# Kernel tuning notes

Hardware: AMD Instinct MI355X
Metric: run time of the kernel (lower is better)

The kernel has to match this reference:

```python
import jax, jax.numpy as jnp
import numpy as np
import math

# Model config (matches init_kwargs)
V, D, H, L, DFF, S_MAX = 32000, 512, 8, 6, 2048, 1024
DK = D // H


def _layernorm(x, g, b, eps=1e-5):
    m = jnp.mean(x, axis=-1, keepdims=True)
    v = jnp.mean(jnp.square(x - m), axis=-1, keepdims=True)
    return (x - m) / jnp.sqrt(v + eps) * g + b


def _pos_encoding(seq_len, d_model):
    # sin on even dims, cos on odd dims
    pos = jnp.arange(seq_len, dtype=jnp.float32)[:, None]          # [S,1]
    div = jnp.exp(jnp.arange(0, d_model, 2, dtype=jnp.float32) *
                  (-math.log(10000.0) / d_model))                   # [D/2]
    ang = pos * div                                                 # [S,D/2]
    pe = jnp.stack([jnp.sin(ang), jnp.cos(ang)], axis=-1)           # [S,D/2,2]
    return pe.reshape(seq_len, d_model)                             # [S,D]


def setup_inputs() -> dict:
    key = jax.random.key(0)
    ks = jax.random.split(key, 24)
    sd = 0.02

    def n(k, shape):
        return jax.random.normal(k, shape, jnp.float32) * sd

    B, S = 2, 1024
    return {
        "tokens": jax.random.randint(ks[0], (B, S), 0, V, dtype=jnp.int32),
        "tok_emb": n(ks[1], (V, D)),
        # attention projections, [L, D, D] stored as (in, out)
        "Wq": n(ks[2], (L, D, D)), "bq": jnp.zeros((L, D)),
        "Wk": n(ks[3], (L, D, D)), "bk": jnp.zeros((L, D)),
        "Wv": n(ks[4], (L, D, D)), "bv": jnp.zeros((L, D)),
        "Wo": n(ks[5], (L, D, D)), "bo": jnp.zeros((L, D)),
        "ln1_g": jnp.ones((L, D)), "ln1_b": jnp.zeros((L, D)),
        "W1": n(ks[6], (L, D, DFF)), "b1": jnp.zeros((L, DFF)),
        "W2": n(ks[7], (L, DFF, D)), "b2": jnp.zeros((L, D)),
        "ln2_g": jnp.ones((L, D)), "ln2_b": jnp.zeros((L, D)),
        "lnf_g": jnp.ones((D,)), "lnf_b": jnp.zeros((D,)),
        "Wout": n(ks[8], (D, V)), "bout": jnp.zeros((V,)),
    }


def reference(tokens, tok_emb, Wq, bq, Wk, bk, Wv, bv, Wo, bo,
              ln1_g, ln1_b, W1, b1, W2, b2, ln2_g, ln2_b,
              lnf_g, lnf_b, Wout, bout):
    B, S = tokens.shape
    x = tok_emb[tokens] * math.sqrt(D) + _pos_encoding(S, D)[None]   # [B,S,D]
    causal = jnp.tril(jnp.ones((S, S), dtype=bool))[None, None]       # [1,1,S,S]
    scale = math.sqrt(DK)

    attns = []
    for l in range(L):
        q = (x @ Wq[l] + bq[l]).reshape(B, S, H, DK).transpose(0, 2, 1, 3)
        k = (x @ Wk[l] + bk[l]).reshape(B, S, H, DK).transpose(0, 2, 1, 3)
        v = (x @ Wv[l] + bv[l]).reshape(B, S, H, DK).transpose(0, 2, 1, 3)
        scores = jnp.einsum('bhsk,bhtk->bhst', q, k) / scale           # [B,H,S,S]
        scores = jnp.where(causal, scores, -1e9)
        a = jax.nn.softmax(scores, axis=-1)
        ctx = jnp.einsum('bhst,bhtk->bhsk', a, v)                      # [B,H,S,DK]
        ctx = ctx.transpose(0, 2, 1, 3).reshape(B, S, D)
        attn_out = ctx @ Wo[l] + bo[l]
        x = _layernorm(x + attn_out, ln1_g[l], ln1_b[l])
        h = jax.nn.gelu(x @ W1[l] + b1[l], approximate=False)          # torch GELU (exact)
        ff = h @ W2[l] + b2[l]
        x = _layernorm(x + ff, ln2_g[l], ln2_b[l])
        attns.append(a)

    x = _layernorm(x, lnf_g, lnf_b)
    logits = x @ Wout + bout                                           # [B,S,V]
    return logits, jnp.stack(attns)                                    # attn: [L,B,H,S,S]
```

## Files before the change

### kernel.cpp

```cpp
#include <hip/hip_runtime.h>
#include <math.h>

#define NB 2
#define NS 1024
#define NH 8
#define NDK 64
#define ND 512
#define NDFF 2048
#define NV 32000
#define NL 6
#define MROWS (NB * NS)
#define QKVLD (3 * ND)

using bf16_t = __bf16;
using bf16x4 = __attribute__((ext_vector_type(4))) __bf16;
using bf16x8 = __attribute__((ext_vector_type(8))) __bf16;
using f32x4  = __attribute__((ext_vector_type(4))) float;

__device__ __forceinline__ void gload_lds16(const bf16_t* g, bf16_t* l) {
  __builtin_amdgcn_global_load_lds(
      (const __attribute__((address_space(1))) void*)g,
      (__attribute__((address_space(3))) void*)l, 16, 0, 0);
}

__device__ __forceinline__ float gelu_exact(float v) {
  return 0.5f * v * (1.0f + erff(v * 0.7071067811865476f));
}

__global__ __launch_bounds__(256)
void prep_kernel(const int* __restrict__ tokens, const float* __restrict__ emb,
                 const float* __restrict__ Wq, const float* __restrict__ Wk,
                 const float* __restrict__ Wv, const float* __restrict__ Wo,
                 const float* __restrict__ W1, const float* __restrict__ W2,
                 const float* __restrict__ Wout,
                 bf16_t* __restrict__ WqkvT, bf16_t* __restrict__ WoT,
                 bf16_t* __restrict__ W1T, bf16_t* __restrict__ W2T,
                 bf16_t* __restrict__ WoutT,
                 float* __restrict__ x, bf16_t* __restrict__ xb) {
  __shared__ bf16_t T[64][72];
  const int id = blockIdx.x;
  const int tid = threadIdx.x;

  if (id >= 8608) {
    const int row = id - 8608;
    const int s = row & (NS - 1);
    const int tok = tokens[row];
    const float SQRTD = 22.627416997969522f;
    const float C = -9.210340371976184f / (float)ND;
#pragma unroll
    for (int i = 0; i < 2; ++i) {
      const int d = tid + i * 256;
      const int pair = d >> 1;
      const float div = expf((float)(2 * pair) * C);
      const float ang = (float)s * div;
      const float pe = (d & 1) ? cosf(ang) : sinf(ang);
      const float v = emb[(size_t)tok * ND + d] * SQRTD + pe;
      x[(size_t)row * ND + d] = v;
      xb[(size_t)row * ND + d] = (bf16_t)v;
    }
    return;
  }

  const float* src; bf16_t* dst; int K, N, n0, k0;
  if (id < 1536) {
    const int z = id >> 6, t = id & 63;
    const int mat = z / 6, layer = z % 6;
    src = ((mat == 0) ? Wq : (mat == 1) ? Wk : (mat == 2) ? Wv : Wo) + (size_t)layer * ND * ND;
    dst = (mat < 3) ? (WqkvT + (size_t)layer * QKVLD * ND + (size_t)mat * ND * ND)
                    : (WoT + (size_t)layer * ND * ND);
    K = ND; N = ND; n0 = (t & 7) * 64; k0 = (t >> 3) * 64;
  } else if (id < 3072) {
    const int idx = id - 1536, layer = idx >> 8, t = idx & 255;
    src = W1 + (size_t)layer * ND * NDFF; dst = W1T + (size_t)layer * NDFF * ND;
    K = ND; N = NDFF; n0 = (t & 31) * 64; k0 = (t >> 5) * 64;
  } else if (id < 4608) {
    const int idx = id - 3072, layer = idx >> 8, t = idx & 255;
    src = W2 + (size_t)layer * NDFF * ND; dst = W2T + (size_t)layer * ND * NDFF;
    K = NDFF; N = ND; n0 = (t & 7) * 64; k0 = (t >> 3) * 64;
  } else {
    const int t = id - 4608;
    src = Wout; dst = WoutT;
    K = ND; N = NV; n0 = (t % 500) * 64; k0 = (t / 500) * 64;
  }

#pragma unroll
  for (int it = 0; it < 4; ++it) {
    const int k = (tid >> 4) + it * 16;
    const int c = (tid & 15) * 4;
    const float4 v = *(const float4*)&src[(size_t)(k0 + k) * N + n0 + c];
    T[c + 0][k] = (bf16_t)v.x;
    T[c + 1][k] = (bf16_t)v.y;
    T[c + 2][k] = (bf16_t)v.z;
    T[c + 3][k] = (bf16_t)v.w;
  }
  __syncthreads();
  const int n = tid >> 2, kk = (tid & 3) * 16;
  bf16x8 a = *(const bf16x8*)&T[n][kk];
  bf16x8 b2v = *(const bf16x8*)&T[n][kk + 8];
  *(bf16x8*)&dst[(size_t)(n0 + n) * K + k0 + kk] = a;
  *(bf16x8*)&dst[(size_t)(n0 + n) * K + k0 + kk + 8] = b2v;
}

__global__ __launch_bounds__(256)
void add_ln_kernel(float* __restrict__ x, const float* __restrict__ y0,
                   const float* __restrict__ y1,
                   const float* __restrict__ g, const float* __restrict__ bb,
                   const float* __restrict__ g2, const float* __restrict__ bb2,
                   bf16_t* __restrict__ xb) {
  const int row = blockIdx.x, tid = threadIdx.x;
  const size_t base = (size_t)row * ND;
  float v0 = x[base + tid], v1 = x[base + tid + 256];
  if (y0) { v0 += y0[base + tid]; v1 += y0[base + tid + 256]; }
  if (y1) { v0 += y1[base + tid]; v1 += y1[base + tid + 256]; }
  __shared__ float red[256];
  red[tid] = v0 + v1; __syncthreads();
  for (int o = 128; o > 0; o >>= 1) {
    if (tid < o) red[tid] += red[tid + o];
    __syncthreads();
  }
  const float mean = red[0] * (1.f / (float)ND);
  __syncthreads();
  const float d0 = v0 - mean, d1 = v1 - mean;
  red[tid] = d0 * d0 + d1 * d1; __syncthreads();
  for (int o = 128; o > 0; o >>= 1) {
    if (tid < o) red[tid] += red[tid + o];
    __syncthreads();
  }
  const float inv = 1.f / sqrtf(red[0] * (1.f / (float)ND) + 1e-5f);
  float o0 = d0 * inv * g[tid]       + bb[tid];
  float o1 = d1 * inv * g[tid + 256] + bb[tid + 256];

  if (g2) {
    __syncthreads();
    red[tid] = o0 + o1; __syncthreads();
    for (int o = 128; o > 0; o >>= 1) {
      if (tid < o) red[tid] += red[tid + o];
      __syncthreads();
    }
    const float mean2 = red[0] * (1.f / (float)ND);
    __syncthreads();
    const float e0 = o0 - mean2, e1 = o1 - mean2;
    red[tid] = e0 * e0 + e1 * e1; __syncthreads();
    for (int o = 128; o > 0; o >>= 1) {
      if (tid < o) red[tid] += red[tid + o];
      __syncthreads();
    }
    const float inv2 = 1.f / sqrtf(red[0] * (1.f / (float)ND) + 1e-5f);
    o0 = e0 * inv2 * g2[tid]       + bb2[tid];
    o1 = e1 * inv2 * g2[tid + 256] + bb2[tid + 256];
  } else {
    x[base + tid] = o0;
    x[base + tid + 256] = o1;
  }
  xb[base + tid] = (bf16_t)o0; xb[base + tid + 256] = (bf16_t)o1;
}

template <int ACT, int OUTBF>
__global__ __launch_bounds__(256)
void gemm_bt(const bf16_t* __restrict__ A, const bf16_t* __restrict__ Wt,
             const float* __restrict__ B0,
             void* __restrict__ Cout, int N, int K, int lda, int ldc) {
  __shared__ bf16_t As[128 * 64];
  __shared__ bf16_t Bs[128 * 64];
  const int tid = threadIdx.x, lane = tid & 63, w = tid >> 6;
  const int wm = w >> 1, wn = w & 1;
  const int lcol = lane & 15, hi = lane >> 4;

  const int nwg = gridDim.x * gridDim.y;
  const int flat = blockIdx.y * gridDim.x + blockIdx.x;
  const int q = nwg >> 3, r = nwg & 7;
  const int xcd = flat & 7, idx = flat >> 3;
  const int nf = (xcd < r ? xcd * (q + 1) : r * (q + 1) + (xcd - r) * q) + idx;
  const int m0 = (nf % gridDim.x) * 128, n0 = (nf / gridDim.x) * 128;

  const int sr8 = lane >> 3;
  const int sslot = lane & 7;

  f32x4 acc[4][4] = {};

  for (int k0 = 0; k0 < K; k0 += 64) {
#pragma unroll
    for (int t = 0; t < 2; ++t) {
#pragma unroll
      for (int c = 0; c < 2; ++c) {
        const int rbase = t * 64 + w * 16 + c * 8;
        const int row = rbase + sr8;
        const int ks = sslot ^ (row & 7);
        gload_lds16(&A[(size_t)(m0 + row) * lda + k0 + ks * 8], &As[rbase * 64]);
        gload_lds16(&Wt[(size_t)(n0 + row) * K + k0 + ks * 8], &Bs[rbase * 64]);
      }
    }
    __syncthreads();

#pragma unroll
    for (int kk = 0; kk < 2; ++kk) {
      bf16x8 af[4], bf[4];
#pragma unroll
      for (int m = 0; m < 4; ++m) {
        const int rr = wm * 64 + m * 16 + lcol;
        af[m] = *(const bf16x8*)&As[rr * 64 + (((kk * 4 + hi) ^ (rr & 7)) * 8)];
      }
#pragma unroll
      for (int n = 0; n < 4; ++n) {
        const int rr = wn * 64 + n * 16 + lcol;
        bf[n] = *(const bf16x8*)&Bs[rr * 64 + (((kk * 4 + hi) ^ (rr & 7)) * 8)];
      }
#pragma unroll
      for (int m = 0; m < 4; ++m)
#pragma unroll
        for (int n = 0; n < 4; ++n)
          acc[m][n] = __builtin_amdgcn_mfma_f32_16x16x32_bf16(bf[n], af[m], acc[m][n], 0, 0, 0);
    }
    __syncthreads();
  }

#pragma unroll
  for (int m = 0; m < 4; ++m) {
    const int row = m0 + wm * 64 + m * 16 + lcol;
#pragma unroll
    for (int n = 0; n < 4; ++n) {
      const int col = n0 + wn * 64 + n * 16 + hi * 4;
      const f32x4 bv = *(const f32x4*)&B0[col];
      f32x4 v;
#pragma unroll
      for (int i = 0; i < 4; ++i) {
        float t = acc[m][n][i] + bv[i];
        if (ACT == 1) t = gelu_exact(t);
        v[i] = t;
      }
      if (OUTBF) {
        bf16x4 o;
#pragma unroll
        for (int i = 0; i < 4; ++i) o[i] = (bf16_t)v[i];
        *(bf16x4*)&((bf16_t*)Cout)[(size_t)row * ldc + col] = o;
      } else {
        __builtin_nontemporal_store(v, (f32x4*)&((float*)Cout)[(size_t)row * ldc + col]);
      }
    }
  }
}

__global__ __launch_bounds__(256)
void gemm_qkv64(const bf16_t* __restrict__ A, const bf16_t* __restrict__ Wt,
                const float* __restrict__ B0, const float* __restrict__ B1,
                const float* __restrict__ B2,
                bf16_t* __restrict__ Cout, int K, int lda, int ldc) {
  __shared__ bf16_t As[64 * 128];
  __shared__ bf16_t Bs[64 * 128];
  const int tid = threadIdx.x, lane = tid & 63, w = tid >> 6;
  const int wm = w >> 1, wn = w & 1;
  const int lcol = lane & 15, hi = lane >> 4;
  const int m0 = blockIdx.x * 64, n0 = blockIdx.y * 64;
  const int sr4 = lane >> 4, sslot = lane & 15;

  f32x4 acc[2][2] = {};

  for (int k0 = 0; k0 < K; k0 += 128) {
#pragma unroll
    for (int c = 0; c < 4; ++c) {
      const int rbase = w * 16 + c * 4;
      const int row = rbase + sr4;
      const int ks = sslot ^ (row & 15);
      gload_lds16(&A[(size_t)(m0 + row) * lda + k0 + ks * 8], &As[rbase * 128]);
      gload_lds16(&Wt[(size_t)(n0 + row) * K + k0 + ks * 8], &Bs[rbase * 128]);
    }
    __syncthreads();

#pragma unroll
    for (int kk = 0; kk < 4; ++kk) {
      bf16x8 af[2], bf[2];
#pragma unroll
      for (int m = 0; m < 2; ++m) {
        const int rr = wm * 32 + m * 16 + lcol;
        af[m] = *(const bf16x8*)&As[rr * 128 + (((kk * 4 + hi) ^ (rr & 15)) * 8)];
      }
#pragma unroll
      for (int n = 0; n < 2; ++n) {
        const int rr = wn * 32 + n * 16 + lcol;
        bf[n] = *(const bf16x8*)&Bs[rr * 128 + (((kk * 4 + hi) ^ (rr & 15)) * 8)];
      }
#pragma unroll
      for (int m = 0; m < 2; ++m)
#pragma unroll
        for (int n = 0; n < 2; ++n)
          acc[m][n] = __builtin_amdgcn_mfma_f32_16x16x32_bf16(bf[n], af[m], acc[m][n], 0, 0, 0);
    }
    __syncthreads();
  }

#pragma unroll
  for (int m = 0; m < 2; ++m) {
    const int row = m0 + wm * 32 + m * 16 + lcol;
#pragma unroll
    for (int n = 0; n < 2; ++n) {
      const int col = n0 + wn * 32 + n * 16 + hi * 4;
      const int sel = col >> 9;
      const float* Bp = (sel == 0) ? B0 : (sel == 1) ? B1 : B2;
      const f32x4 bv = *(const f32x4*)&Bp[col & 511];
      bf16x4 o;
#pragma unroll
      for (int i = 0; i < 4; ++i) o[i] = (bf16_t)(acc[m][n][i] + bv[i]);
      *(bf16x4*)&Cout[(size_t)row * ldc + col] = o;
    }
  }
}

template <int ACT, int OUTBF>
__global__ __launch_bounds__(256)
void gemm64(const bf16_t* __restrict__ A, const bf16_t* __restrict__ Wt,
            const float* __restrict__ bias,
            void* __restrict__ Cout, int K, int lda, int ldw, int kmask,
            int ldc, size_t zstride) {
  __shared__ bf16_t As[64 * 128];
  __shared__ bf16_t Bs[64 * 128];
  const int tid = threadIdx.x, lane = tid & 63, w = tid >> 6;
  const int wm = w >> 1, wn = w & 1;
  const int lcol = lane & 15, hi = lane >> 4;
  const int m0 = blockIdx.x * 64, n0 = blockIdx.y * 64;
  const int sr4 = lane >> 4, sslot = lane & 15;
  const int kc = K / gridDim.z;
  const int kbeg = blockIdx.z * kc;

  f32x4 acc[2][2] = {};

  for (int k0 = kbeg; k0 < kbeg + kc; k0 += 128) {
#pragma unroll
    for (int c = 0; c < 4; ++c) {
      const int rbase = w * 16 + c * 4;
      const int row = rbase + sr4;
      const int ks = sslot ^ (row & 15);
      gload_lds16(&A[(size_t)(m0 + row) * lda + k0 + ks * 8], &As[rbase * 128]);
      gload_lds16(&Wt[(size_t)(n0 + row) * ldw + ((k0 & kmask) + ks * 8)], &Bs[rbase * 128]);
    }
    __syncthreads();

#pragma unroll
    for (int kk = 0; kk < 4; ++kk) {
      bf16x8 af[2], bf[2];
#pragma unroll
      for (int m = 0; m < 2; ++m) {
        const int rr = wm * 32 + m * 16 + lcol;
        af[m] = *(const bf16x8*)&As[rr * 128 + (((kk * 4 + hi) ^ (rr & 15)) * 8)];
      }
#pragma unroll
      for (int n = 0; n < 2; ++n) {
        const int rr = wn * 32 + n * 16 + lcol;
        bf[n] = *(const bf16x8*)&Bs[rr * 128 + (((kk * 4 + hi) ^ (rr & 15)) * 8)];
      }
#pragma unroll
      for (int m = 0; m < 2; ++m)
#pragma unroll
        for (int n = 0; n < 2; ++n)
          acc[m][n] = __builtin_amdgcn_mfma_f32_16x16x32_bf16(bf[n], af[m], acc[m][n], 0, 0, 0);
    }
    __syncthreads();
  }

#pragma unroll
  for (int m = 0; m < 2; ++m) {
    const int row = m0 + wm * 32 + m * 16 + lcol;
#pragma unroll
    for (int n = 0; n < 2; ++n) {
      const int col = n0 + wn * 32 + n * 16 + hi * 4;
      f32x4 bv = {0.f, 0.f, 0.f, 0.f};
      if (blockIdx.z == 0) bv = *(const f32x4*)&bias[col];
      f32x4 v;
#pragma unroll
      for (int i = 0; i < 4; ++i) {
        float t = acc[m][n][i] + bv[i];
        if (ACT == 1) t = gelu_exact(t);
        v[i] = t;
      }
      if (OUTBF) {
        bf16x4 o;
#pragma unroll
        for (int i = 0; i < 4; ++i) o[i] = (bf16_t)v[i];
        *(bf16x4*)&((bf16_t*)Cout)[(size_t)row * ldc + col] = o;
      } else {
        *(f32x4*)&((float*)Cout)[blockIdx.z * zstride + (size_t)row * ldc + col] = v;
      }
    }
  }
}

__global__ __launch_bounds__(256)
void attn_stats(const bf16_t* __restrict__ qkv,
                float* __restrict__ marr, float* __restrict__ sarr) {
  const int qt = 15 - blockIdx.x;
  const int h = blockIdx.y;
  const int b = blockIdx.z >> 1, half = blockIdx.z & 1;
  const int q0 = qt * 64;
  const int NTT = (q0 >> 7) + 1;
  const int qmax = q0 + 63;
  const int tid = threadIdx.x, lane = tid & 63, wq = tid >> 6;
  const int lcol = lane & 15, hi = lane >> 4;

  __shared__ bf16_t Qs[64][72];
  __shared__ bf16_t Ks[128][72];

  {
    const int r = tid >> 2, c = (tid & 3) * 16;
    const bf16_t* src = &qkv[((size_t)(b * NS + q0 + r)) * QKVLD + h * NDK + c];
    *(bf16x8*)&Qs[r][c]     = *(const bf16x8*)&src[0];
    *(bf16x8*)&Qs[r][c + 8] = *(const bf16x8*)&src[8];
  }
  __syncthreads();
  const bf16x8 qf0 = *(const bf16x8*)&Qs[wq * 16 + lcol][hi * 8];
  const bf16x8 qf1 = *(const bf16x8*)&Qs[wq * 16 + lcol][32 + hi * 8];
  const int qrow = q0 + wq * 16 + lcol;
  const float scale = 0.125f;

  float m_run = -1e30f, s_run = 0.f;

  for (int tt = half; tt < NTT; tt += 2) {
    const int t0 = tt * 128;
    const int fmax = min(8, ((qmax - t0) >> 4) + 1);
    {
      const int r = tid >> 1, cb = (tid & 1) * 32;
      const bf16_t* src = &qkv[((size_t)(b * NS + t0 + r)) * QKVLD + ND + h * NDK + cb];
#pragma unroll
      for (int j = 0; j < 4; ++j)
        *(bf16x8*)&Ks[r][cb + j * 8] = *(const bf16x8*)&src[j * 8];
    }
    __syncthreads();

    float tmax = -1e30f;
    f32x4 sc[8];
#pragma unroll
    for (int f = 0; f < 8; ++f) {
      if (f >= fmax) break;
      f32x4 s4 = {};
      const bf16x8 ka0 = *(const bf16x8*)&Ks[f * 16 + lcol][hi * 8];
      const bf16x8 ka1 = *(const bf16x8*)&Ks[f * 16 + lcol][32 + hi * 8];
      s4 = __builtin_amdgcn_mfma_f32_16x16x32_bf16(ka0, qf0, s4, 0, 0, 0);
      s4 = __builtin_amdgcn_mfma_f32_16x16x32_bf16(ka1, qf1, s4, 0, 0, 0);
#pragma unroll
      for (int i = 0; i < 4; ++i) {
        const int t = t0 + f * 16 + hi * 4 + i;
        const float v = (t <= qrow) ? s4[i] * scale : -1e30f;
        s4[i] = v;
        tmax = fmaxf(tmax, v);
      }
      sc[f] = s4;
    }
    tmax = fmaxf(tmax, __shfl_xor(tmax, 16));
    tmax = fmaxf(tmax, __shfl_xor(tmax, 32));
    const float m_new = fmaxf(m_run, tmax);
    float sum = 0.f;
#pragma unroll
    for (int f = 0; f < 8; ++f) {
      if (f >= fmax) break;
#pragma unroll
      for (int i = 0; i < 4; ++i) sum += __expf(sc[f][i] - m_new);
    }
    sum += __shfl_xor(sum, 16);
    sum += __shfl_xor(sum, 32);
    s_run = s_run * __expf(m_run - m_new) + sum;
    m_run = m_new;
    __syncthreads();
  }

  if (hi == 0) {
    const size_t idx = (((size_t)half * NB + b) * NH + h) * NS + qrow;
    marr[idx] = m_run;
    sarr[idx] = s_run;
  }
}

__global__ __launch_bounds__(256)
void attn_pv(const bf16_t* __restrict__ qkv,
             const float* __restrict__ marr, const float* __restrict__ sarr,
             float* __restrict__ probs, bf16_t* __restrict__ ctxcat) {
  const int qt = 15 - blockIdx.x;
  const int h = blockIdx.y;
  const int b = blockIdx.z >> 1, half = blockIdx.z & 1;
  const int q0 = qt * 64;
  const int NTT = (q0 >> 7) + 1;
  const int qmax = q0 + 63;
  const int tid = threadIdx.x, lane = tid & 63, wq = tid >> 6;
  const int lcol = lane & 15, hi = lane >> 4;

  __shared__ bf16_t Qs[64][72];
  __shared__ bf16_t Ks[128][72];
  __shared__ bf16_t Vs[64][132];
  __shared__ bf16_t Ps[64][132];

  if (half == 0) {
    const int z0 = NTT * 128;
    const int nz = (NS - z0) >> 2;
    if (nz > 0) {
      const f32x4 zf = {0.f, 0.f, 0.f, 0.f};
      for (int idx = tid; idx < 64 * nz; idx += 256) {
        const int r = idx / nz, c = (idx - r * nz) * 4;
        __builtin_nontemporal_store(zf,
            (f32x4*)&probs[(((size_t)b * NH + h) * NS + q0 + r) * NS + z0 + c]);
      }
    }
  }

  {
    const int r = tid >> 2, c = (tid & 3) * 16;
    const bf16_t* src = &qkv[((size_t)(b * NS + q0 + r)) * QKVLD + h * NDK + c];
    *(bf16x8*)&Qs[r][c]     = *(const bf16x8*)&src[0];
    *(bf16x8*)&Qs[r][c + 8] = *(const bf16x8*)&src[8];
  }
  __syncthreads();
  const bf16x8 qf0 = *(const bf16x8*)&Qs[wq * 16 + lcol][hi * 8];
  const bf16x8 qf1 = *(const bf16x8*)&Qs[wq * 16 + lcol][32 + hi * 8];
  const int qrow = q0 + wq * 16 + lcol;
  const float scale = 0.125f;

  const size_t i0 = (((size_t)0 * NB + b) * NH + h) * NS + qrow;
  const size_t i1 = (((size_t)1 * NB + b) * NH + h) * NS + qrow;
  const float m0 = marr[i0], m1 = marr[i1];
  const float s0 = sarr[i0], s1 = sarr[i1];
  const float m_fin = fmaxf(m0, m1);
  const float s_fin = s0 * __expf(m0 - m_fin) + s1 * __expf(m1 - m_fin);
  const float inv = 1.f / s_fin;

  f32x4 cacc[4] = {};
  const size_t prow = (((size_t)b * NH + h) * NS + qrow) * NS;
  for (int tt = half; tt < NTT; tt += 2) {
    const int t0 = tt * 128;
    const int fmax = min(8, ((qmax - t0) >> 4) + 1);
    {
      const int r = tid >> 1, cb = (tid & 1) * 32;
      const bf16_t* src = &qkv[((size_t)(b * NS + t0 + r)) * QKVLD + ND + h * NDK + cb];
#pragma unroll
      for (int j = 0; j < 4; ++j)
        *(bf16x8*)&Ks[r][cb + j * 8] = *(const bf16x8*)&src[j * 8];
    }
    {
#pragma unroll
      for (int it = 0; it < 2; ++it) {
        const int t4 = (tid >> 4) * 4 + it * 64;
        const int dk4 = (tid & 15) * 4;
        bf16x4 rr[4];
#pragma unroll
        for (int i = 0; i < 4; ++i)
          rr[i] = *(const bf16x4*)&qkv[((size_t)(b * NS + t0 + t4 + i)) * QKVLD + 2 * ND + h * NDK + dk4];
#pragma unroll
        for (int j = 0; j < 4; ++j) {
          bf16x4 c;
#pragma unroll
          for (int i = 0; i < 4; ++i) c[i] = rr[i][j];
          *(bf16x4*)&Vs[dk4 + j][t4] = c;
        }
      }
    }
    __syncthreads();

    const f32x4 zf = {0.f, 0.f, 0.f, 0.f};
    const bf16x4 zb = {(bf16_t)0.f, (bf16_t)0.f, (bf16_t)0.f, (bf16_t)0.f};
#pragma unroll
    for (int f = 0; f < 8; ++f) {
      if (f < fmax) {
        f32x4 s4 = {};
        const bf16x8 ka0 = *(const bf16x8*)&Ks[f * 16 + lcol][hi * 8];
        const bf16x8 ka1 = *(const bf16x8*)&Ks[f * 16 + lcol][32 + hi * 8];
        s4 = __builtin_amdgcn_mfma_f32_16x16x32_bf16(ka0, qf0, s4, 0, 0, 0);
        s4 = __builtin_amdgcn_mfma_f32_16x16x32_bf16(ka1, qf1, s4, 0, 0, 0);
        f32x4 pw;
        bf16x4 pb;
#pragma unroll
        for (int i = 0; i < 4; ++i) {
          const int t = t0 + f * 16 + hi * 4 + i;
          const float v = (t <= qrow) ? s4[i] * scale : -1e30f;
          const float pr = __expf(v - m_fin) * inv;
          pw[i] = pr;
          pb[i] = (bf16_t)pr;
        }
        __builtin_nontemporal_store(pw, (f32x4*)&probs[prow + t0 + f * 16 + hi * 4]);
        *(bf16x4*)&Ps[wq * 16 + lcol][f * 16 + hi * 4] = pb;
      } else {
        __builtin_nontemporal_store(zf, (f32x4*)&probs[prow + t0 + f * 16 + hi * 4]);
        *(bf16x4*)&Ps[wq * 16 + lcol][f * 16 + hi * 4] = zb;
      }
    }

#pragma unroll
    for (int ks = 0; ks < 4; ++ks) {
      const bf16x8 pf = *(const bf16x8*)&Ps[wq * 16 + lcol][ks * 32 + hi * 8];
#pragma unroll
      for (int df = 0; df < 4; ++df) {
        const bf16x8 vf = *(const bf16x8*)&Vs[df * 16 + lcol][ks * 32 + hi * 8];
        cacc[df] = __builtin_amdgcn_mfma_f32_16x16x32_bf16(vf, pf, cacc[df], 0, 0, 0);
      }
    }
    __syncthreads();
  }

#pragma unroll
  for (int df = 0; df < 4; ++df) {
    bf16x4 o;
#pragma unroll
    for (int i = 0; i < 4; ++i) o[i] = (bf16_t)cacc[df][i];
    *(bf16x4*)&ctxcat[((size_t)(b * NS + qrow)) * 1024 + half * 512 + h * NDK + df * 16 + hi * 4] = o;
  }
}

extern "C" void kernel_launch(void* const* d_in, const int* in_sizes, int n_in,
                              void* d_out, int out_size, void* d_ws, size_t ws_size,
                              hipStream_t stream) {
  const int*   tokens  = (const int*)d_in[0];
  const float* tok_emb = (const float*)d_in[1];
  const float* Wq = (const float*)d_in[2];
  const float* bq = (const float*)d_in[3];
  const float* Wk = (const float*)d_in[4];
  const float* bk = (const float*)d_in[5];
  const float* Wv = (const float*)d_in[6];
  const float* bv = (const float*)d_in[7];
  const float* Wo = (const float*)d_in[8];
  const float* bo = (const float*)d_in[9];
  const float* ln1_g = (const float*)d_in[10];
  const float* ln1_b = (const float*)d_in[11];
  const float* W1 = (const float*)d_in[12];
  const float* b1 = (const float*)d_in[13];
  const float* W2 = (const float*)d_in[14];
  const float* b2 = (const float*)d_in[15];
  const float* ln2_g = (const float*)d_in[16];
  const float* ln2_b = (const float*)d_in[17];
  const float* lnf_g = (const float*)d_in[18];
  const float* lnf_b = (const float*)d_in[19];
  const float* Wout = (const float*)d_in[20];
  const float* bout = (const float*)d_in[21];

  float* logits   = (float*)d_out;
  float* attn_all = (float*)d_out + (size_t)NB * NS * NV;

  char* w = (char*)d_ws;
  float* x    = (float*)w;  w += (size_t)4 << 20;
  float* tmp  = (float*)w;  w += (size_t)8 << 20;
  bf16_t* xb  = (bf16_t*)w; w += (size_t)2 << 20;
  bf16_t* qkv = (bf16_t*)w; w += (size_t)6 << 20;
  float* marr = (float*)w;
  float* sarr = (float*)(w + (512 << 10));
  w += (size_t)2 << 20;
  bf16_t* hh  = (bf16_t*)w;
  bf16_t* ctxcat = (bf16_t*)w;
  w += (size_t)8 << 20;
  bf16_t* WqkvT = (bf16_t*)w; w += (size_t)6 * QKVLD * ND * 2;
  bf16_t* WoT   = (bf16_t*)w; w += (size_t)6 * ND * ND * 2;
  bf16_t* W1T   = (bf16_t*)w; w += (size_t)6 * NDFF * ND * 2;
  bf16_t* W2T   = (bf16_t*)w; w += (size_t)6 * ND * NDFF * 2;
  bf16_t* WoutT = (bf16_t*)w; w += (size_t)NV * ND * 2;
  if ((size_t)(w - (char*)d_ws) > ws_size) return;

  const int M = MROWS;
  const size_t U = (size_t)M * ND;
  float* tmp1 = tmp + U;

  prep_kernel<<<10656, 256, 0, stream>>>(tokens, tok_emb, Wq, Wk, Wv, Wo, W1, W2, Wout,
                                         WqkvT, WoT, W1T, W2T, WoutT, x, xb);

  const dim3 gQKV(M / 64, QKVLD / 64);
  const dim3 gFF1(M / 64, NDFF / 64);
  const dim3 gOut(M / 128, NV / 128);
  const dim3 g64s(M / 64, ND / 64, 2);
  const dim3 gAttn(16, NH, NB * 2);

  const int ALLK = 0x7fffffff;

  for (int l = 0; l < NL; ++l) {
    gemm_qkv64<<<gQKV, 256, 0, stream>>>(xb, WqkvT + (size_t)l * QKVLD * ND,
        bq + l * ND, bk + l * ND, bv + l * ND, qkv, ND, ND, QKVLD);

    float* probs_l = attn_all + (size_t)l * NB * NH * NS * NS;
    attn_stats<<<gAttn, 256, 0, stream>>>(qkv, marr, sarr);
    attn_pv<<<gAttn, 256, 0, stream>>>(qkv, marr, sarr, probs_l, ctxcat);

    gemm64<0, 0><<<g64s, 256, 0, stream>>>(ctxcat, WoT + (size_t)l * ND * ND,
        bo + l * ND, tmp, 1024, 1024, ND, 511, ND, U);
    add_ln_kernel<<<M, 256, 0, stream>>>(x, tmp, tmp1,
        ln1_g + l * ND, ln1_b + l * ND, nullptr, nullptr, xb);

    gemm64<1, 1><<<gFF1, 256, 0, stream>>>(xb, W1T + (size_t)l * NDFF * ND,
        b1 + l * NDFF, hh, ND, ND, ND, ALLK, NDFF, 0);
    gemm64<0, 0><<<g64s, 256, 0, stream>>>(hh, W2T + (size_t)l * ND * NDFF,
        b2 + l * ND, tmp, NDFF, NDFF, NDFF, ALLK, ND, U);
    add_ln_kernel<<<M, 256, 0, stream>>>(x, tmp, tmp1,
        ln2_g + l * ND, ln2_b + l * ND,
        (l == NL - 1) ? lnf_g : nullptr, (l == NL - 1) ? lnf_b : nullptr, xb);
  }

  gemm_bt<0, 0><<<gOut, 256, 0, stream>>>(xb, WoutT, bout,
      logits, NV, ND, ND, NV);
}
```

Measured before the change: 649.4 us.

## Split attention key range four ways and move zero-fill into stats kernel

Attention stats and PV kernels now split the causal key tiles across four partitions instead of two, doubling the grid to raise occupancy for the short triangular workloads. The final softmax stats merge four partial max/sum pairs. Partial contexts are written into a 4x512-wide concat buffer that the Wo GEMM reduces via a K of 2048. The zero-filling of masked probability entries moves from the PV kernel into the stats kernel, and shared memory is trimmed by aliasing Q staging into the K/V buffers. More partitions add redundant Q loads and a larger Wo GEMM K dimension.

```diff
diff --git a/kernel.cpp b/kernel.cpp
--- a/kernel.cpp
+++ b/kernel.cpp
@@ -385,107 +385,20 @@
 
 __global__ __launch_bounds__(256)
 void attn_stats(const bf16_t* __restrict__ qkv,
-                float* __restrict__ marr, float* __restrict__ sarr) {
+                float* __restrict__ marr, float* __restrict__ sarr,
+                float* __restrict__ probs) {
   const int qt = 15 - blockIdx.x;
   const int h = blockIdx.y;
-  const int b = blockIdx.z >> 1, half = blockIdx.z & 1;
+  const int b = blockIdx.z >> 2, quar = blockIdx.z & 3;
   const int q0 = qt * 64;
   const int NTT = (q0 >> 7) + 1;
   const int qmax = q0 + 63;
   const int tid = threadIdx.x, lane = tid & 63, wq = tid >> 6;
   const int lcol = lane & 15, hi = lane >> 4;
 
-  __shared__ bf16_t Qs[64][72];
   __shared__ bf16_t Ks[128][72];
 
-  {
-    const int r = tid >> 2, c = (tid & 3) * 16;
-    const bf16_t* src = &qkv[((size_t)(b * NS + q0 + r)) * QKVLD + h * NDK + c];
-    *(bf16x8*)&Qs[r][c]     = *(const bf16x8*)&src[0];
-    *(bf16x8*)&Qs[r][c + 8] = *(const bf16x8*)&src[8];
-  }
-  __syncthreads();
-  const bf16x8 qf0 = *(const bf16x8*)&Qs[wq * 16 + lcol][hi * 8];
-  const bf16x8 qf1 = *(const bf16x8*)&Qs[wq * 16 + lcol][32 + hi * 8];
-  const int qrow = q0 + wq * 16 + lcol;
-  const float scale = 0.125f;
-
-  float m_run = -1e30f, s_run = 0.f;
-
-  for (int tt = half; tt < NTT; tt += 2) {
-    const int t0 = tt * 128;
-    const int fmax = min(8, ((qmax - t0) >> 4) + 1);
-    {
-      const int r = tid >> 1, cb = (tid & 1) * 32;
-      const bf16_t* src = &qkv[((size_t)(b * NS + t0 + r)) * QKVLD + ND + h * NDK + cb];
-#pragma unroll
-      for (int j = 0; j < 4; ++j)
-        *(bf16x8*)&Ks[r][cb + j * 8] = *(const bf16x8*)&src[j * 8];
-    }
-    __syncthreads();
-
-    float tmax = -1e30f;
-    f32x4 sc[8];
-#pragma unroll
-    for (int f = 0; f < 8; ++f) {
-      if (f >= fmax) break;
-      f32x4 s4 = {};
-      const bf16x8 ka0 = *(const bf16x8*)&Ks[f * 16 + lcol][hi * 8];
-      const bf16x8 ka1 = *(const bf16x8*)&Ks[f * 16 + lcol][32 + hi * 8];
-      s4 = __builtin_amdgcn_mfma_f32_16x16x32_bf16(ka0, qf0, s4, 0, 0, 0);
-      s4 = __builtin_amdgcn_mfma_f32_16x16x32_bf16(ka1, qf1, s4, 0, 0, 0);
-#pragma unroll
-      for (int i = 0; i < 4; ++i) {
-        const int t = t0 + f * 16 + hi * 4 + i;
-        const float v = (t <= qrow) ? s4[i] * scale : -1e30f;
-        s4[i] = v;
-        tmax = fmaxf(tmax, v);
-      }
-      sc[f] = s4;
-    }
-    tmax = fmaxf(tmax, __shfl_xor(tmax, 16));
-    tmax = fmaxf(tmax, __shfl_xor(tmax, 32));
-    const float m_new = fmaxf(m_run, tmax);
-    float sum = 0.f;
-#pragma unroll
-    for (int f = 0; f < 8; ++f) {
-      if (f >= fmax) break;
-#pragma unroll
-      for (int i = 0; i < 4; ++i) sum += __expf(sc[f][i] - m_new);
-    }
-    sum += __shfl_xor(sum, 16);
-    sum += __shfl_xor(sum, 32);
-    s_run = s_run * __expf(m_run - m_new) + sum;
-    m_run = m_new;
-    __syncthreads();
-  }
-
-  if (hi == 0) {
-    const size_t idx = (((size_t)half * NB + b) * NH + h) * NS + qrow;
-    marr[idx] = m_run;
-    sarr[idx] = s_run;
-  }
-}
-
-__global__ __launch_bounds__(256)
-void attn_pv(const bf16_t* __restrict__ qkv,
-             const float* __restrict__ marr, const float* __restrict__ sarr,
-             float* __restrict__ probs, bf16_t* __restrict__ ctxcat) {
-  const int qt = 15 - blockIdx.x;
-  const int h = blockIdx.y;
-  const int b = blockIdx.z >> 1, half = blockIdx.z & 1;
-  const int q0 = qt * 64;
-  const int NTT = (q0 >> 7) + 1;
-  const int qmax = q0 + 63;
-  const int tid = threadIdx.x, lane = tid & 63, wq = tid >> 6;
-  const int lcol = lane & 15, hi = lane >> 4;
-
-  __shared__ bf16_t Qs[64][72];
-  __shared__ bf16_t Ks[128][72];
-  __shared__ bf16_t Vs[64][132];
-  __shared__ bf16_t Ps[64][132];
-
-  if (half == 0) {
+  if (quar == 0) {
     const int z0 = NTT * 128;
     const int nz = (NS - z0) >> 2;
     if (nz > 0) {
@@ -501,26 +414,119 @@
   {
     const int r = tid >> 2, c = (tid & 3) * 16;
     const bf16_t* src = &qkv[((size_t)(b * NS + q0 + r)) * QKVLD + h * NDK + c];
+    *(bf16x8*)&Ks[r][c]     = *(const bf16x8*)&src[0];
+    *(bf16x8*)&Ks[r][c + 8] = *(const bf16x8*)&src[8];
+  }
+  __syncthreads();
+  const bf16x8 qf0 = *(const bf16x8*)&Ks[wq * 16 + lcol][hi * 8];
+  const bf16x8 qf1 = *(const bf16x8*)&Ks[wq * 16 + lcol][32 + hi * 8];
+  __syncthreads();
+  const int qrow = q0 + wq * 16 + lcol;
+  const float scale = 0.125f;
+
+  float m_run = -1e30f, s_run = 0.f;
+
+  for (int tt = quar; tt < NTT; tt += 4) {
+    const int t0 = tt * 128;
+    const int fmax = min(8, ((qmax - t0) >> 4) + 1);
+    {
+      const int r = tid >> 1, cb = (tid & 1) * 32;
+      const bf16_t* src = &qkv[((size_t)(b * NS + t0 + r)) * QKVLD + ND + h * NDK + cb];
+#pragma unroll
+      for (int j = 0; j < 4; ++j)
+        *(bf16x8*)&Ks[r][cb + j * 8] = *(const bf16x8*)&src[j * 8];
+    }
+    __syncthreads();
+
+    float tmax = -1e30f;
+    f32x4 sc[8];
+#pragma unroll
+    for (int f = 0; f < 8; ++f) {
+      if (f >= fmax) break;
+      f32x4 s4 = {};
+      const bf16x8 ka0 = *(const bf16x8*)&Ks[f * 16 + lcol][hi * 8];
+      const bf16x8 ka1 = *(const bf16x8*)&Ks[f * 16 + lcol][32 + hi * 8];
+      s4 = __builtin_amdgcn_mfma_f32_16x16x32_bf16(ka0, qf0, s4, 0, 0, 0);
+      s4 = __builtin_amdgcn_mfma_f32_16x16x32_bf16(ka1, qf1, s4, 0, 0, 0);
+#pragma unroll
+      for (int i = 0; i < 4; ++i) {
+        const int t = t0 + f * 16 + hi * 4 + i;
+        const float v = (t <= qrow) ? s4[i] * scale : -1e30f;
+        s4[i] = v;
+        tmax = fmaxf(tmax, v);
+      }
+      sc[f] = s4;
+    }
+    tmax = fmaxf(tmax, __shfl_xor(tmax, 16));
+    tmax = fmaxf(tmax, __shfl_xor(tmax, 32));
+    const float m_new = fmaxf(m_run, tmax);
+    float sum = 0.f;
+#pragma unroll
+    for (int f = 0; f < 8; ++f) {
+      if (f >= fmax) break;
+#pragma unroll
+      for (int i = 0; i < 4; ++i) sum += __expf(sc[f][i] - m_new);
+    }
+    sum += __shfl_xor(sum, 16);
+    sum += __shfl_xor(sum, 32);
+    s_run = s_run * __expf(m_run - m_new) + sum;
+    m_run = m_new;
+    __syncthreads();
+  }
+
+  if (hi == 0) {
+    const size_t idx = (((size_t)quar * NB + b) * NH + h) * NS + qrow;
+    marr[idx] = m_run;
+    sarr[idx] = s_run;
+  }
+}
+
+__global__ __launch_bounds__(256)
+void attn_pv(const bf16_t* __restrict__ qkv,
+             const float* __restrict__ marr, const float* __restrict__ sarr,
+             float* __restrict__ probs, bf16_t* __restrict__ ctxcat) {
+  const int qt = 15 - blockIdx.x;
+  const int h = blockIdx.y;
+  const int b = blockIdx.z >> 2, quar = blockIdx.z & 3;
+  const int q0 = qt * 64;
+  const int NTT = (q0 >> 7) + 1;
+  const int qmax = q0 + 63;
+  const int tid = threadIdx.x, lane = tid & 63, wq = tid >> 6;
+  const int lcol = lane & 15, hi = lane >> 4;
+
+  __shared__ bf16_t Ks[128][72];
+  __shared__ bf16_t Vs[64][132];
+  __shared__ bf16_t Ps[64][132];
+  bf16_t (*Qs)[72] = (bf16_t(*)[72])&Vs[0][0];
+
+  {
+    const int r = tid >> 2, c = (tid & 3) * 16;
+    const bf16_t* src = &qkv[((size_t)(b * NS + q0 + r)) * QKVLD + h * NDK + c];
     *(bf16x8*)&Qs[r][c]     = *(const bf16x8*)&src[0];
     *(bf16x8*)&Qs[r][c + 8] = *(const bf16x8*)&src[8];
   }
   __syncthreads();
   const bf16x8 qf0 = *(const bf16x8*)&Qs[wq * 16 + lcol][hi * 8];
   const bf16x8 qf1 = *(const bf16x8*)&Qs[wq * 16 + lcol][32 + hi * 8];
+  __syncthreads();
   const int qrow = q0 + wq * 16 + lcol;
   const float scale = 0.125f;
 
-  const size_t i0 = (((size_t)0 * NB + b) * NH + h) * NS + qrow;
-  const size_t i1 = (((size_t)1 * NB + b) * NH + h) * NS + qrow;
-  const float m0 = marr[i0], m1 = marr[i1];
-  const float s0 = sarr[i0], s1 = sarr[i1];
-  const float m_fin = fmaxf(m0, m1);
-  const float s_fin = s0 * __expf(m0 - m_fin) + s1 * __expf(m1 - m_fin);
+  float mq0, mq1, mq2, mq3, sq0, sq1, sq2, sq3;
+  {
+    const size_t strideq = (size_t)NB * NH * NS;
+    const size_t i0 = (((size_t)b * NH + h) * NS) + qrow;
+    mq0 = marr[i0]; mq1 = marr[i0 + strideq]; mq2 = marr[i0 + 2 * strideq]; mq3 = marr[i0 + 3 * strideq];
+    sq0 = sarr[i0]; sq1 = sarr[i0 + strideq]; sq2 = sarr[i0 + 2 * strideq]; sq3 = sarr[i0 + 3 * strideq];
+  }
+  const float m_fin = fmaxf(fmaxf(mq0, mq1), fmaxf(mq2, mq3));
+  const float s_fin = sq0 * __expf(mq0 - m_fin) + sq1 * __expf(mq1 - m_fin) +
+                      sq2 * __expf(mq2 - m_fin) + sq3 * __expf(mq3 - m_fin);
   const float inv = 1.f / s_fin;
 
   f32x4 cacc[4] = {};
   const size_t prow = (((size_t)b * NH + h) * NS + qrow) * NS;
-  for (int tt = half; tt < NTT; tt += 2) {
+  for (int tt = quar; tt < NTT; tt += 4) {
     const int t0 = tt * 128;
     const int fmax = min(8, ((qmax - t0) >> 4) + 1);
     {
@@ -595,7 +601,7 @@
     bf16x4 o;
 #pragma unroll
     for (int i = 0; i < 4; ++i) o[i] = (bf16_t)cacc[df][i];
-    *(bf16x4*)&ctxcat[((size_t)(b * NS + qrow)) * 1024 + half * 512 + h * NDK + df * 16 + hi * 4] = o;
+    *(bf16x4*)&ctxcat[((size_t)(b * NS + qrow)) * 2048 + quar * 512 + h * NDK + df * 16 + hi * 4] = o;
   }
 }
 
@@ -634,7 +640,7 @@
   bf16_t* xb  = (bf16_t*)w; w += (size_t)2 << 20;
   bf16_t* qkv = (bf16_t*)w; w += (size_t)6 << 20;
   float* marr = (float*)w;
-  float* sarr = (float*)(w + (512 << 10));
+  float* sarr = (float*)(w + (1 << 20));
   w += (size_t)2 << 20;
   bf16_t* hh  = (bf16_t*)w;
   bf16_t* ctxcat = (bf16_t*)w;
@@ -657,7 +663,7 @@
   const dim3 gFF1(M / 64, NDFF / 64);
   const dim3 gOut(M / 128, NV / 128);
   const dim3 g64s(M / 64, ND / 64, 2);
-  const dim3 gAttn(16, NH, NB * 2);
+  const dim3 gAttn(16, NH, NB * 4);
 
   const int ALLK = 0x7fffffff;
 
@@ -666,11 +672,11 @@
         bq + l * ND, bk + l * ND, bv + l * ND, qkv, ND, ND, QKVLD);
 
     float* probs_l = attn_all + (size_t)l * NB * NH * NS * NS;
-    attn_stats<<<gAttn, 256, 0, stream>>>(qkv, marr, sarr);
+    attn_stats<<<gAttn, 256, 0, stream>>>(qkv, marr, sarr, probs_l);
     attn_pv<<<gAttn, 256, 0, stream>>>(qkv, marr, sarr, probs_l, ctxcat);
 
     gemm64<0, 0><<<g64s, 256, 0, stream>>>(ctxcat, WoT + (size_t)l * ND * ND,
-        bo + l * ND, tmp, 1024, 1024, ND, 511, ND, U);
+        bo + l * ND, tmp, 2048, 2048, ND, 511, ND, U);
     add_ln_kernel<<<M, 256, 0, stream>>>(x, tmp, tmp1,
         ln1_g + l * ND, ln1_b + l * ND, nullptr, nullptr, xb);
 
```

After: 675.2 us. +4.0%, slower.
